# Optimization experiments

Measured on AMD Instinct MI355X. Metric: run time of the kernel, lower is better.

Reference implementation:

```python
import jax, jax.numpy as jnp
import numpy as np

B = 64        # number of jagged segments
LMAX = 1024   # max_seq_len
D = 512       # input feature dim
K = 512       # output feature dim
NW = 128      # number of selectable weight matrices
T = 32768     # total jagged tokens (avg len 512)


def setup_inputs() -> dict:
    rng = np.random.default_rng(0)
    # Monotone offsets with avg segment length T//B = 512, jittered +/-200
    # so every length stays in (0, LMAX].
    offsets = np.arange(B + 1, dtype=np.int64) * (T // B)
    offsets[1:-1] += rng.integers(-200, 200, size=B - 1)
    key = jax.random.key(0)
    k1, k2, k3, k4 = jax.random.split(key, 4)
    jagged = jax.random.normal(k1, (T, D), dtype=jnp.float32)
    weight = jax.random.normal(k2, (NW, D, K), dtype=jnp.float32) * 0.02
    bias = jax.random.normal(k3, (NW, K), dtype=jnp.float32)
    index = jax.random.randint(k4, (B,), 0, NW)
    return {
        "max_seq_len": LMAX,
        "offsets": jnp.asarray(offsets),
        "index": index,
        "jagged": jagged,
        "weight": weight,
        "bias": bias,
    }


def reference(max_seq_len, offsets, index, jagged, weight, bias):
    # out[offsets[b]:offsets[b+1]] = jagged[offsets[b]:offsets[b+1]] @ weight[index[b]] + bias[index[b]]
    T_, Dd = jagged.shape
    Kk = weight.shape[-1]
    starts = offsets[:-1]            # [B]
    ends = offsets[1:]               # [B]
    pos = starts[:, None] + jnp.arange(max_seq_len)[None, :]   # [B, L] global row ids
    valid = pos < ends[:, None]                                # [B, L]
    safe = jnp.where(valid, pos, 0)
    padded = jnp.where(valid[..., None], jagged[safe], 0)      # [B, L, D]
    w = weight[index]                                          # [B, D, K] (index-select)
    b = bias[index]                                            # [B, K]
    out_p = jnp.einsum("bld,bdk->blk", padded, w) + b[:, None, :]  # [B, L, K]
    # Scatter padded result back to jagged layout; invalid slots go to row T_ (dropped).
    scatter_idx = jnp.where(valid, pos, T_)
    out = jnp.zeros((T_ + 1, Kk), jagged.dtype).at[scatter_idx].set(out_p)
    return out[:T_]
```

## Files before the change

kernel.cpp:

```cpp
#include <hip/hip_runtime.h>
#include <hip/hip_bf16.h>

#define D_DIM 512
#define K_DIM 512
#define B_C   64
#define LMAX_C 1024

#define BM 128
#define BN 128
#define BK 64
#define KSTEPS 8
#define ROWT 8
#define COLT 4
#define NWG  (B_C * ROWT * COLT)

typedef __attribute__((ext_vector_type(8))) short bf16x8;
typedef __attribute__((ext_vector_type(4))) float f32x4;

__device__ __forceinline__ short f2bf(float f) {
    union { __hip_bfloat16 h; short s; } u;
    u.h = __float2bfloat16(f);
    return u.s;
}

__device__ __forceinline__ short* lds_addr(short* base, int row, int kbyte) {
    return (short*)((char*)base + row * 128 +
                    (kbyte ^ ((((row & 7) ^ ((row >> 2) & 7))) << 4)));
}

__global__ __launch_bounds__(256, 2) void jbmm_kernel(
    const int* __restrict__ offsets,
    const int* __restrict__ index,
    const float* __restrict__ jagged,
    const float* __restrict__ weight,
    const float* __restrict__ bias,
    float* __restrict__ out)
{
    __shared__ short As[2][BM * BK];
    __shared__ short Bs[2][BN * BK];

    const int bidRaw = blockIdx.x;
    const int bid = (bidRaw & 7) * (NWG / 8) + (bidRaw >> 3);

    const int b   = bid / (ROWT * COLT);
    const int rt  = (bid / COLT) % ROWT;
    const int ct  = bid % COLT;

    const int start = offsets[b];
    const int end   = offsets[b + 1];
    const int m0    = start + rt * BM;
    if (m0 >= end) return;
    const int rows = (end - m0) < BM ? (end - m0) : BM;

    const int idxw = index[b];
    const float* W = weight + (size_t)idxw * D_DIM * K_DIM;
    const int n0 = ct * BN;

    const int tid  = threadIdx.x;
    const int lane = tid & 63;
    const int wid  = tid >> 6;
    const int wr   = wid >> 1;
    const int wc   = wid & 1;
    const int lr   = lane & 15;
    const int lg   = lane >> 4;

    const int arow  = tid >> 3;
    const int acol8 = tid & 7;
    const int n4    = tid & 31;
    const int dq8   = tid >> 5;

    float bias_v[4];
#pragma unroll
    for (int ni = 0; ni < 4; ++ni)
        bias_v[ni] = bias[(size_t)idxw * K_DIM + n0 + wc * 64 + ni * 16 + lr];

    f32x4 acc[4][4];
#pragma unroll
    for (int mi = 0; mi < 4; ++mi)
#pragma unroll
        for (int ni = 0; ni < 4; ++ni)
            acc[mi][ni] = (f32x4){0.f, 0.f, 0.f, 0.f};

    f32x4 aR[8];
    f32x4 bR[8];

#define LOADA(k0_)                                                          \
    {                                                                       \
        _Pragma("unroll")                                                   \
        for (int i = 0; i < 4; ++i) {                                       \
            const int r = arow + 32 * i;                                    \
            f32x4 v0 = (f32x4){0.f,0.f,0.f,0.f};                            \
            f32x4 v1 = (f32x4){0.f,0.f,0.f,0.f};                            \
            if (r < rows) {                                                 \
                const float* p = &jagged[(size_t)(m0 + r) * D_DIM + (k0_) + acol8 * 8]; \
                v0 = *reinterpret_cast<const f32x4*>(p);                    \
                v1 = *reinterpret_cast<const f32x4*>(p + 4);                \
            }                                                               \
            aR[2 * i] = v0; aR[2 * i + 1] = v1;                             \
        }                                                                   \
    }

#define LOADB(k0_)                                                          \
    {                                                                       \
        _Pragma("unroll")                                                   \
        for (int j = 0; j < 8; ++j)                                         \
            bR[j] = *reinterpret_cast<const f32x4*>(                        \
                &W[(size_t)((k0_) + dq8 * 8 + j) * K_DIM + n0 + n4 * 4]);   \
    }

#define CVTSTORE(c_)                                                        \
    {                                                                       \
        _Pragma("unroll")                                                   \
        for (int i = 0; i < 4; ++i) {                                       \
            const int r = arow + 32 * i;                                    \
            bf16x8 w;                                                       \
            w[0] = f2bf(aR[2*i][0]); w[1] = f2bf(aR[2*i][1]);               \
            w[2] = f2bf(aR[2*i][2]); w[3] = f2bf(aR[2*i][3]);               \
            w[4] = f2bf(aR[2*i+1][0]); w[5] = f2bf(aR[2*i+1][1]);           \
            w[6] = f2bf(aR[2*i+1][2]); w[7] = f2bf(aR[2*i+1][3]);           \
            *reinterpret_cast<bf16x8*>(lds_addr(&As[c_][0], r, acol8 * 16)) = w; \
        }                                                                   \
        _Pragma("unroll")                                                   \
        for (int np = 0; np < 4; ++np) {                                    \
            bf16x8 w;                                                       \
            w[0] = f2bf(bR[0][np]); w[1] = f2bf(bR[1][np]);                 \
            w[2] = f2bf(bR[2][np]); w[3] = f2bf(bR[3][np]);                 \
            w[4] = f2bf(bR[4][np]); w[5] = f2bf(bR[5][np]);                 \
            w[6] = f2bf(bR[6][np]); w[7] = f2bf(bR[7][np]);                 \
            *reinterpret_cast<bf16x8*>(lds_addr(&Bs[c_][0], n4 * 4 + np, dq8 * 16)) = w; \
        }                                                                   \
    }

#define COMPUTE(c_)                                                         \
    {                                                                       \
        __builtin_amdgcn_s_setprio(1);                                      \
        _Pragma("unroll")                                                   \
        for (int kh = 0; kh < 2; ++kh) {                                    \
            bf16x8 af[4], bfr[4];                                           \
            _Pragma("unroll")                                               \
            for (int mi = 0; mi < 4; ++mi)                                  \
                af[mi] = *reinterpret_cast<bf16x8*>(                        \
                    lds_addr(&As[c_][0], wr * 64 + mi * 16 + lr, kh * 64 + lg * 16)); \
            _Pragma("unroll")                                               \
            for (int ni = 0; ni < 4; ++ni)                                  \
                bfr[ni] = *reinterpret_cast<bf16x8*>(                       \
                    lds_addr(&Bs[c_][0], wc * 64 + ni * 16 + lr, kh * 64 + lg * 16)); \
            _Pragma("unroll")                                               \
            for (int mi = 0; mi < 4; ++mi)                                  \
                _Pragma("unroll")                                           \
                for (int ni = 0; ni < 4; ++ni)                              \
                    acc[mi][ni] = __builtin_amdgcn_mfma_f32_16x16x32_bf16(  \
                        af[mi], bfr[ni], acc[mi][ni], 0, 0, 0);             \
        }                                                                   \
        __builtin_amdgcn_s_setprio(0);                                      \
    }

#define BARRIER_LDS()                                                       \
    {                                                                       \
        asm volatile("s_waitcnt lgkmcnt(0)" ::: "memory");                  \
        __builtin_amdgcn_s_barrier();                                       \
        asm volatile("" ::: "memory");                                      \
    }

    LOADA(0); LOADB(0);
    CVTSTORE(0);
    BARRIER_LDS();

#pragma unroll
    for (int t = 0; t < KSTEPS; ++t) {
        if (t + 1 < KSTEPS) {
            const int kn = (t + 1) * BK;
            LOADA(kn); LOADB(kn);
        }
        COMPUTE(t & 1);
        if (t + 1 < KSTEPS) {
            CVTSTORE((t + 1) & 1);
            BARRIER_LDS();
        }
    }

#pragma unroll
    for (int mi = 0; mi < 4; ++mi) {
        const int rloc = wr * 64 + mi * 16 + lg * 4;
#pragma unroll
        for (int r = 0; r < 4; ++r) {
            const int rr = rloc + r;
            if (rr < rows) {
#pragma unroll
                for (int ni = 0; ni < 4; ++ni) {
                    out[(size_t)(m0 + rr) * K_DIM + n0 + wc * 64 + ni * 16 + lr] =
                        acc[mi][ni][r] + bias_v[ni];
                }
            }
        }
    }
}

extern "C" void kernel_launch(void* const* d_in, const int* in_sizes, int n_in,
                              void* d_out, int out_size, void* d_ws, size_t ws_size,
                              hipStream_t stream) {
    const int*   offsets = (const int*)d_in[1];
    const int*   index   = (const int*)d_in[2];
    const float* jagged  = (const float*)d_in[3];
    const float* weight  = (const float*)d_in[4];
    const float* bias    = (const float*)d_in[5];
    float*       out     = (float*)d_out;

    dim3 grid(NWG);
    dim3 block(256);
    hipLaunchKernelGGL(jbmm_kernel, grid, block, 0, stream,
                       offsets, index, jagged, weight, bias, out);
}
```

Before: 46.56 us.

## Keep per-segment weight slice resident in LDS and loop over row tiles

Each workgroup now owns one (segment, column-tile) pair. It converts the full 512x128 weight slice to bf16 once into a 128KB LDS buffer, then loops over all row tiles of the segment, streaming only the activations through a double buffer. This removes the repeated fp32 weight loads and conversions that every row tile used to do. Block size goes to 512 threads, each wave owning a 64x32 output sub-tile. The cost is a grid of only 256 large workgroups with roughly 160KB of LDS each, so one fits per CU. Uneven segment lengths now become serial per-block imbalance, and there is less parallelism for hiding latency.

```diff
diff --git a/kernel.cpp b/kernel.cpp
--- a/kernel.cpp
+++ b/kernel.cpp
@@ -4,7 +4,6 @@
 #define D_DIM 512
 #define K_DIM 512
 #define B_C   64
-#define LMAX_C 1024
 
 #define BM 128
 #define BN 128
@@ -12,7 +11,7 @@
 #define KSTEPS 8
 #define ROWT 8
 #define COLT 4
-#define NWG  (B_C * ROWT * COLT)
+#define NWG  (B_C * COLT)
 
 typedef __attribute__((ext_vector_type(8))) short bf16x8;
 typedef __attribute__((ext_vector_type(4))) float f32x4;
@@ -23,12 +22,10 @@
     return u.s;
 }
 
-__device__ __forceinline__ short* lds_addr(short* base, int row, int kbyte) {
-    return (short*)((char*)base + row * 128 +
-                    (kbyte ^ ((((row & 7) ^ ((row >> 2) & 7))) << 4)));
-}
-
-__global__ __launch_bounds__(256, 2) void jbmm_kernel(
+__device__ __forceinline__ int fA(int r) { return (r & 7) ^ ((r >> 2) & 7); }
+__device__ __forceinline__ int fW(int r) { return (r & 15) ^ ((r >> 2) & 15); }
+
+__global__ __launch_bounds__(512, 2) void jbmm_kernel(
     const int* __restrict__ offsets,
     const int* __restrict__ index,
     const float* __restrict__ jagged,
@@ -36,119 +33,118 @@
     const float* __restrict__ bias,
     float* __restrict__ out)
 {
+    __shared__ short Ws[BN * D_DIM];
     __shared__ short As[2][BM * BK];
-    __shared__ short Bs[2][BN * BK];
 
     const int bidRaw = blockIdx.x;
     const int bid = (bidRaw & 7) * (NWG / 8) + (bidRaw >> 3);
-
-    const int b   = bid / (ROWT * COLT);
-    const int rt  = (bid / COLT) % ROWT;
-    const int ct  = bid % COLT;
+    const int b  = bid >> 2;
+    const int ct = bid & 3;
 
     const int start = offsets[b];
     const int end   = offsets[b + 1];
-    const int m0    = start + rt * BM;
-    if (m0 >= end) return;
-    const int rows = (end - m0) < BM ? (end - m0) : BM;
-
-    const int idxw = index[b];
-    const float* W = weight + (size_t)idxw * D_DIM * K_DIM;
-    const int n0 = ct * BN;
+    const int idxw  = index[b];
+    const int n0    = ct * BN;
+    const float* W  = weight + (size_t)idxw * D_DIM * K_DIM;
 
     const int tid  = threadIdx.x;
     const int lane = tid & 63;
     const int wid  = tid >> 6;
-    const int wr   = wid >> 1;
-    const int wc   = wid & 1;
+    const int wr   = wid >> 2;
+    const int wc   = wid & 3;
     const int lr   = lane & 15;
     const int lg   = lane >> 4;
 
-    const int arow  = tid >> 3;
-    const int acol8 = tid & 7;
-    const int n4    = tid & 31;
-    const int dq8   = tid >> 5;
-
-    float bias_v[4];
-#pragma unroll
-    for (int ni = 0; ni < 4; ++ni)
-        bias_v[ni] = bias[(size_t)idxw * K_DIM + n0 + wc * 64 + ni * 16 + lr];
-
-    f32x4 acc[4][4];
-#pragma unroll
-    for (int mi = 0; mi < 4; ++mi)
-#pragma unroll
-        for (int ni = 0; ni < 4; ++ni)
-            acc[mi][ni] = (f32x4){0.f, 0.f, 0.f, 0.f};
-
-    f32x4 aR[8];
-    f32x4 bR[8];
+    {
+        const int nq = tid & 31;
+        const int kg = tid >> 5;
+        for (int p = 0; p < 4; ++p) {
+            const int kbase = p * 128;
+            f32x4 wv[8];
+#pragma unroll
+            for (int j = 0; j < 8; ++j)
+                wv[j] = *reinterpret_cast<const f32x4*>(
+                    &W[(size_t)(kbase + kg * 8 + j) * K_DIM + n0 + nq * 4]);
+#pragma unroll
+            for (int np = 0; np < 4; ++np) {
+                const int row = nq * 4 + np;
+                bf16x8 w8;
+                w8[0] = f2bf(wv[0][np]); w8[1] = f2bf(wv[1][np]);
+                w8[2] = f2bf(wv[2][np]); w8[3] = f2bf(wv[3][np]);
+                w8[4] = f2bf(wv[4][np]); w8[5] = f2bf(wv[5][np]);
+                w8[6] = f2bf(wv[6][np]); w8[7] = f2bf(wv[7][np]);
+                const int sp = (p * 16 + kg) ^ fW(row);
+                *reinterpret_cast<bf16x8*>((char*)Ws + row * 1024 + sp * 16) = w8;
+            }
+        }
+    }
+
+    float bias_v[2];
+#pragma unroll
+    for (int ni = 0; ni < 2; ++ni)
+        bias_v[ni] = bias[(size_t)idxw * K_DIM + n0 + wc * 32 + ni * 16 + lr];
+
+    asm volatile("s_waitcnt lgkmcnt(0)" ::: "memory");
+    __builtin_amdgcn_s_barrier();
+    asm volatile("" ::: "memory");
+
+    const int arow  = tid >> 2;
+    const int acol4 = tid & 3;
+
+    f32x4 aR[4];
 
 #define LOADA(k0_)                                                          \
     {                                                                       \
+        if (arow < rows) {                                                  \
+            const float* p = &jagged[(size_t)(m0 + arow) * D_DIM + (k0_) + acol4 * 16]; \
+            _Pragma("unroll")                                               \
+            for (int j = 0; j < 4; ++j)                                     \
+                aR[j] = *reinterpret_cast<const f32x4*>(p + 4 * j);         \
+        } else {                                                            \
+            _Pragma("unroll")                                               \
+            for (int j = 0; j < 4; ++j)                                     \
+                aR[j] = (f32x4){0.f, 0.f, 0.f, 0.f};                        \
+        }                                                                   \
+    }
+
+#define CVTSTORE_A(c_)                                                      \
+    {                                                                       \
         _Pragma("unroll")                                                   \
-        for (int i = 0; i < 4; ++i) {                                       \
-            const int r = arow + 32 * i;                                    \
-            f32x4 v0 = (f32x4){0.f,0.f,0.f,0.f};                            \
-            f32x4 v1 = (f32x4){0.f,0.f,0.f,0.f};                            \
-            if (r < rows) {                                                 \
-                const float* p = &jagged[(size_t)(m0 + r) * D_DIM + (k0_) + acol8 * 8]; \
-                v0 = *reinterpret_cast<const f32x4*>(p);                    \
-                v1 = *reinterpret_cast<const f32x4*>(p + 4);                \
-            }                                                               \
-            aR[2 * i] = v0; aR[2 * i + 1] = v1;                             \
+        for (int j2 = 0; j2 < 2; ++j2) {                                    \
+            bf16x8 w8;                                                      \
+            w8[0] = f2bf(aR[2*j2][0]);   w8[1] = f2bf(aR[2*j2][1]);         \
+            w8[2] = f2bf(aR[2*j2][2]);   w8[3] = f2bf(aR[2*j2][3]);         \
+            w8[4] = f2bf(aR[2*j2+1][0]); w8[5] = f2bf(aR[2*j2+1][1]);       \
+            w8[6] = f2bf(aR[2*j2+1][2]); w8[7] = f2bf(aR[2*j2+1][3]);       \
+            const int sp = (acol4 * 2 + j2) ^ fA(arow);                     \
+            *reinterpret_cast<bf16x8*>((char*)&As[c_][0] + arow * 128 + sp * 16) = w8; \
         }                                                                   \
     }
 
-#define LOADB(k0_)                                                          \
-    {                                                                       \
-        _Pragma("unroll")                                                   \
-        for (int j = 0; j < 8; ++j)                                         \
-            bR[j] = *reinterpret_cast<const f32x4*>(                        \
-                &W[(size_t)((k0_) + dq8 * 8 + j) * K_DIM + n0 + n4 * 4]);   \
-    }
-
-#define CVTSTORE(c_)                                                        \
-    {                                                                       \
-        _Pragma("unroll")                                                   \
-        for (int i = 0; i < 4; ++i) {                                       \
-            const int r = arow + 32 * i;                                    \
-            bf16x8 w;                                                       \
-            w[0] = f2bf(aR[2*i][0]); w[1] = f2bf(aR[2*i][1]);               \
-            w[2] = f2bf(aR[2*i][2]); w[3] = f2bf(aR[2*i][3]);               \
-            w[4] = f2bf(aR[2*i+1][0]); w[5] = f2bf(aR[2*i+1][1]);           \
-            w[6] = f2bf(aR[2*i+1][2]); w[7] = f2bf(aR[2*i+1][3]);           \
-            *reinterpret_cast<bf16x8*>(lds_addr(&As[c_][0], r, acol8 * 16)) = w; \
-        }                                                                   \
-        _Pragma("unroll")                                                   \
-        for (int np = 0; np < 4; ++np) {                                    \
-            bf16x8 w;                                                       \
-            w[0] = f2bf(bR[0][np]); w[1] = f2bf(bR[1][np]);                 \
-            w[2] = f2bf(bR[2][np]); w[3] = f2bf(bR[3][np]);                 \
-            w[4] = f2bf(bR[4][np]); w[5] = f2bf(bR[5][np]);                 \
-            w[6] = f2bf(bR[6][np]); w[7] = f2bf(bR[7][np]);                 \
-            *reinterpret_cast<bf16x8*>(lds_addr(&Bs[c_][0], n4 * 4 + np, dq8 * 16)) = w; \
-        }                                                                   \
-    }
-
-#define COMPUTE(c_)                                                         \
+#define COMPUTE(c_, t_)                                                     \
     {                                                                       \
         __builtin_amdgcn_s_setprio(1);                                      \
         _Pragma("unroll")                                                   \
         for (int kh = 0; kh < 2; ++kh) {                                    \
-            bf16x8 af[4], bfr[4];                                           \
-            _Pragma("unroll")                                               \
-            for (int mi = 0; mi < 4; ++mi)                                  \
+            bf16x8 af[4], bfr[2];                                           \
+            _Pragma("unroll")                                               \
+            for (int mi = 0; mi < 4; ++mi) {                                \
+                const int row = wr * 64 + mi * 16 + lr;                     \
+                const int sp = (kh * 4 + lg) ^ fA(row);                     \
                 af[mi] = *reinterpret_cast<bf16x8*>(                        \
-                    lds_addr(&As[c_][0], wr * 64 + mi * 16 + lr, kh * 64 + lg * 16)); \
-            _Pragma("unroll")                                               \
-            for (int ni = 0; ni < 4; ++ni)                                  \
+                    (char*)&As[c_][0] + row * 128 + sp * 16);               \
+            }                                                               \
+            _Pragma("unroll")                                               \
+            for (int ni = 0; ni < 2; ++ni) {                                \
+                const int row = wc * 32 + ni * 16 + lr;                     \
+                const int sp = ((t_) * 8 + kh * 4 + lg) ^ fW(row);          \
                 bfr[ni] = *reinterpret_cast<bf16x8*>(                       \
-                    lds_addr(&Bs[c_][0], wc * 64 + ni * 16 + lr, kh * 64 + lg * 16)); \
+                    (char*)Ws + row * 1024 + sp * 16);                      \
+            }                                                               \
             _Pragma("unroll")                                               \
             for (int mi = 0; mi < 4; ++mi)                                  \
                 _Pragma("unroll")                                           \
-                for (int ni = 0; ni < 4; ++ni)                              \
+                for (int ni = 0; ni < 2; ++ni)                              \
                     acc[mi][ni] = __builtin_amdgcn_mfma_f32_16x16x32_bf16(  \
                         af[mi], bfr[ni], acc[mi][ni], 0, 0, 0);             \
         }                                                                   \
@@ -162,34 +158,43 @@
         asm volatile("" ::: "memory");                                      \
     }
 
-    LOADA(0); LOADB(0);
-    CVTSTORE(0);
-    BARRIER_LDS();
-
-#pragma unroll
-    for (int t = 0; t < KSTEPS; ++t) {
-        if (t + 1 < KSTEPS) {
-            const int kn = (t + 1) * BK;
-            LOADA(kn); LOADB(kn);
+    for (int rt = 0; rt < ROWT; ++rt) {
+        const int m0 = start + rt * BM;
+        if (m0 >= end) break;
+        const int rows = (end - m0) < BM ? (end - m0) : BM;
+
+        f32x4 acc[4][2];
+#pragma unroll
+        for (int mi = 0; mi < 4; ++mi)
+#pragma unroll
+            for (int ni = 0; ni < 2; ++ni)
+                acc[mi][ni] = (f32x4){0.f, 0.f, 0.f, 0.f};
+
+        LOADA(0);
+        CVTSTORE_A(0);
+        BARRIER_LDS();
+
+#pragma unroll
+        for (int t = 0; t < KSTEPS; ++t) {
+            if (t + 1 < KSTEPS) LOADA((t + 1) * BK);
+            COMPUTE(t & 1, t);
+            if (t + 1 < KSTEPS) {
+                CVTSTORE_A((t + 1) & 1);
+                BARRIER_LDS();
+            }
         }
-        COMPUTE(t & 1);
-        if (t + 1 < KSTEPS) {
-            CVTSTORE((t + 1) & 1);
-            BARRIER_LDS();
-        }
-    }
-
-#pragma unroll
-    for (int mi = 0; mi < 4; ++mi) {
-        const int rloc = wr * 64 + mi * 16 + lg * 4;
-#pragma unroll
-        for (int r = 0; r < 4; ++r) {
-            const int rr = rloc + r;
-            if (rr < rows) {
-#pragma unroll
-                for (int ni = 0; ni < 4; ++ni) {
-                    out[(size_t)(m0 + rr) * K_DIM + n0 + wc * 64 + ni * 16 + lr] =
-                        acc[mi][ni][r] + bias_v[ni];
+
+#pragma unroll
+        for (int mi = 0; mi < 4; ++mi) {
+            const int rbase = wr * 64 + mi * 16 + lg * 4;
+#pragma unroll
+            for (int r = 0; r < 4; ++r) {
+                const int rr = rbase + r;
+                if (rr < rows) {
+#pragma unroll
+                    for (int ni = 0; ni < 2; ++ni)
+                        out[(size_t)(m0 + rr) * K_DIM + n0 + wc * 32 + ni * 16 + lr] =
+                            acc[mi][ni][r] + bias_v[ni];
                 }
             }
         }
@@ -207,7 +212,7 @@
     float*       out     = (float*)d_out;
 
     dim3 grid(NWG);
-    dim3 block(256);
+    dim3 block(512);
     hipLaunchKernelGGL(jbmm_kernel, grid, block, 0, stream,
                        offsets, index, jagged, weight, bias, out);
 }
```

Result: slower. 68.47 us (+47.0%).

## Halve BK, deepen register prefetch to two stages, raise occupancy to three

Applied to the files above, without the earlier changes.

Cuts the K tile from 64 to 32 and doubles the number of K steps. Global loads now run two steps ahead, using a double-buffered register stage on top of the double-buffered LDS. The smaller LDS footprint allows launch_bounds occupancy of 3 blocks per CU, and a new 64-byte-row swizzle plus narrower load and store vectors fit the new tile shape. The aim is better latency hiding of the fp32 loads, at the cost of twice as many barriers, smaller vector loads for W, and more register pressure.

```diff
diff --git a/kernel.cpp b/kernel.cpp
--- a/kernel.cpp
+++ b/kernel.cpp
@@ -4,18 +4,19 @@
 #define D_DIM 512
 #define K_DIM 512
 #define B_C   64
-#define LMAX_C 1024
 
 #define BM 128
 #define BN 128
-#define BK 64
-#define KSTEPS 8
+#define BK 32
+#define KSTEPS 16
 #define ROWT 8
 #define COLT 4
 #define NWG  (B_C * ROWT * COLT)
 
 typedef __attribute__((ext_vector_type(8))) short bf16x8;
+typedef __attribute__((ext_vector_type(4))) short bf16x4;
 typedef __attribute__((ext_vector_type(4))) float f32x4;
+typedef __attribute__((ext_vector_type(2))) float f32x2;
 
 __device__ __forceinline__ short f2bf(float f) {
     union { __hip_bfloat16 h; short s; } u;
@@ -23,12 +24,11 @@
     return u.s;
 }
 
-__device__ __forceinline__ short* lds_addr(short* base, int row, int kbyte) {
-    return (short*)((char*)base + row * 128 +
-                    (kbyte ^ ((((row & 7) ^ ((row >> 2) & 7))) << 4)));
-}
-
-__global__ __launch_bounds__(256, 2) void jbmm_kernel(
+__device__ __forceinline__ char* lds_addr(short* base, int row, int slot, int byte_in_slot) {
+    return (char*)base + row * 64 + ((slot ^ ((row >> 1) & 3)) << 4) + byte_in_slot;
+}
+
+__global__ __launch_bounds__(256, 3) void jbmm_kernel(
     const int* __restrict__ offsets,
     const int* __restrict__ index,
     const float* __restrict__ jagged,
@@ -64,10 +64,10 @@
     const int lr   = lane & 15;
     const int lg   = lane >> 4;
 
-    const int arow  = tid >> 3;
-    const int acol8 = tid & 7;
-    const int n4    = tid & 31;
-    const int dq8   = tid >> 5;
+    const int arow = tid >> 3;
+    const int aq   = tid & 7;
+    const int wnp  = tid & 63;
+    const int wko  = tid >> 6;
 
     float bias_v[4];
 #pragma unroll
@@ -81,77 +81,72 @@
         for (int ni = 0; ni < 4; ++ni)
             acc[mi][ni] = (f32x4){0.f, 0.f, 0.f, 0.f};
 
-    f32x4 aR[8];
-    f32x4 bR[8];
-
-#define LOADA(k0_)                                                          \
+    f32x4 aR[2][4];
+    f32x2 bR[2][8];
+
+#define LOADA(k0_, s_)                                                      \
     {                                                                       \
         _Pragma("unroll")                                                   \
         for (int i = 0; i < 4; ++i) {                                       \
             const int r = arow + 32 * i;                                    \
-            f32x4 v0 = (f32x4){0.f,0.f,0.f,0.f};                            \
-            f32x4 v1 = (f32x4){0.f,0.f,0.f,0.f};                            \
-            if (r < rows) {                                                 \
-                const float* p = &jagged[(size_t)(m0 + r) * D_DIM + (k0_) + acol8 * 8]; \
-                v0 = *reinterpret_cast<const f32x4*>(p);                    \
-                v1 = *reinterpret_cast<const f32x4*>(p + 4);                \
-            }                                                               \
-            aR[2 * i] = v0; aR[2 * i + 1] = v1;                             \
+            f32x4 v = (f32x4){0.f, 0.f, 0.f, 0.f};                          \
+            if (r < rows)                                                   \
+                v = *reinterpret_cast<const f32x4*>(                        \
+                    &jagged[(size_t)(m0 + r) * D_DIM + (k0_) + aq * 4]);    \
+            aR[s_][i] = v;                                                  \
         }                                                                   \
     }
 
-#define LOADB(k0_)                                                          \
-    {                                                                       \
-        _Pragma("unroll")                                                   \
-        for (int j = 0; j < 8; ++j)                                         \
-            bR[j] = *reinterpret_cast<const f32x4*>(                        \
-                &W[(size_t)((k0_) + dq8 * 8 + j) * K_DIM + n0 + n4 * 4]);   \
-    }
-
-#define CVTSTORE(c_)                                                        \
+#define LOADB(k0_, s_)                                                      \
+    {                                                                       \
+        _Pragma("unroll")                                                   \
+        for (int jj = 0; jj < 8; ++jj)                                      \
+            bR[s_][jj] = *reinterpret_cast<const f32x2*>(                   \
+                &W[(size_t)((k0_) + wko * 8 + jj) * K_DIM + n0 + wnp * 2]); \
+    }
+
+#define CVTSTORE(s_, c_)                                                    \
     {                                                                       \
         _Pragma("unroll")                                                   \
         for (int i = 0; i < 4; ++i) {                                       \
             const int r = arow + 32 * i;                                    \
-            bf16x8 w;                                                       \
-            w[0] = f2bf(aR[2*i][0]); w[1] = f2bf(aR[2*i][1]);               \
-            w[2] = f2bf(aR[2*i][2]); w[3] = f2bf(aR[2*i][3]);               \
-            w[4] = f2bf(aR[2*i+1][0]); w[5] = f2bf(aR[2*i+1][1]);           \
-            w[6] = f2bf(aR[2*i+1][2]); w[7] = f2bf(aR[2*i+1][3]);           \
-            *reinterpret_cast<bf16x8*>(lds_addr(&As[c_][0], r, acol8 * 16)) = w; \
+            bf16x4 w4;                                                      \
+            w4[0] = f2bf(aR[s_][i][0]); w4[1] = f2bf(aR[s_][i][1]);         \
+            w4[2] = f2bf(aR[s_][i][2]); w4[3] = f2bf(aR[s_][i][3]);         \
+            *reinterpret_cast<bf16x4*>(                                     \
+                lds_addr(&As[c_][0], r, aq >> 1, (aq & 1) * 8)) = w4;       \
         }                                                                   \
         _Pragma("unroll")                                                   \
-        for (int np = 0; np < 4; ++np) {                                    \
-            bf16x8 w;                                                       \
-            w[0] = f2bf(bR[0][np]); w[1] = f2bf(bR[1][np]);                 \
-            w[2] = f2bf(bR[2][np]); w[3] = f2bf(bR[3][np]);                 \
-            w[4] = f2bf(bR[4][np]); w[5] = f2bf(bR[5][np]);                 \
-            w[6] = f2bf(bR[6][np]); w[7] = f2bf(bR[7][np]);                 \
-            *reinterpret_cast<bf16x8*>(lds_addr(&Bs[c_][0], n4 * 4 + np, dq8 * 16)) = w; \
+        for (int j = 0; j < 2; ++j) {                                       \
+            const int rb = wnp * 2 + j;                                     \
+            bf16x8 w8;                                                      \
+            w8[0] = f2bf(bR[s_][0][j]); w8[1] = f2bf(bR[s_][1][j]);         \
+            w8[2] = f2bf(bR[s_][2][j]); w8[3] = f2bf(bR[s_][3][j]);         \
+            w8[4] = f2bf(bR[s_][4][j]); w8[5] = f2bf(bR[s_][5][j]);         \
+            w8[6] = f2bf(bR[s_][6][j]); w8[7] = f2bf(bR[s_][7][j]);         \
+            *reinterpret_cast<bf16x8*>(                                     \
+                lds_addr(&Bs[c_][0], rb, wko, 0)) = w8;                     \
         }                                                                   \
     }
 
 #define COMPUTE(c_)                                                         \
     {                                                                       \
         __builtin_amdgcn_s_setprio(1);                                      \
-        _Pragma("unroll")                                                   \
-        for (int kh = 0; kh < 2; ++kh) {                                    \
-            bf16x8 af[4], bfr[4];                                           \
-            _Pragma("unroll")                                               \
-            for (int mi = 0; mi < 4; ++mi)                                  \
-                af[mi] = *reinterpret_cast<bf16x8*>(                        \
-                    lds_addr(&As[c_][0], wr * 64 + mi * 16 + lr, kh * 64 + lg * 16)); \
+        bf16x8 af[4], bfr[4];                                               \
+        _Pragma("unroll")                                                   \
+        for (int mi = 0; mi < 4; ++mi)                                      \
+            af[mi] = *reinterpret_cast<bf16x8*>(                            \
+                lds_addr(&As[c_][0], wr * 64 + mi * 16 + lr, lg, 0));       \
+        _Pragma("unroll")                                                   \
+        for (int ni = 0; ni < 4; ++ni)                                      \
+            bfr[ni] = *reinterpret_cast<bf16x8*>(                           \
+                lds_addr(&Bs[c_][0], wc * 64 + ni * 16 + lr, lg, 0));       \
+        _Pragma("unroll")                                                   \
+        for (int mi = 0; mi < 4; ++mi)                                      \
             _Pragma("unroll")                                               \
             for (int ni = 0; ni < 4; ++ni)                                  \
-                bfr[ni] = *reinterpret_cast<bf16x8*>(                       \
-                    lds_addr(&Bs[c_][0], wc * 64 + ni * 16 + lr, kh * 64 + lg * 16)); \
-            _Pragma("unroll")                                               \
-            for (int mi = 0; mi < 4; ++mi)                                  \
-                _Pragma("unroll")                                           \
-                for (int ni = 0; ni < 4; ++ni)                              \
-                    acc[mi][ni] = __builtin_amdgcn_mfma_f32_16x16x32_bf16(  \
-                        af[mi], bfr[ni], acc[mi][ni], 0, 0, 0);             \
-        }                                                                   \
+                acc[mi][ni] = __builtin_amdgcn_mfma_f32_16x16x32_bf16(      \
+                    af[mi], bfr[ni], acc[mi][ni], 0, 0, 0);                 \
         __builtin_amdgcn_s_setprio(0);                                      \
     }
 
@@ -162,19 +157,20 @@
         asm volatile("" ::: "memory");                                      \
     }
 
-    LOADA(0); LOADB(0);
-    CVTSTORE(0);
+    LOADA(0, 0); LOADB(0, 0);
+    LOADA(BK, 1); LOADB(BK, 1);
+    CVTSTORE(0, 0);
     BARRIER_LDS();
 
 #pragma unroll
     for (int t = 0; t < KSTEPS; ++t) {
-        if (t + 1 < KSTEPS) {
-            const int kn = (t + 1) * BK;
-            LOADA(kn); LOADB(kn);
+        if (t + 2 < KSTEPS) {
+            const int kn = (t + 2) * BK;
+            LOADA(kn, t & 1); LOADB(kn, t & 1);
         }
         COMPUTE(t & 1);
         if (t + 1 < KSTEPS) {
-            CVTSTORE((t + 1) & 1);
+            CVTSTORE((t + 1) & 1, (t + 1) & 1);
             BARRIER_LDS();
         }
     }
```

New measurement: 97.03 us. +108.4%, slower.

## Widen N tile to 256 and switch to single-buffered LDS staging

Applied to the files above, without the earlier changes.

Doubles the output tile width per workgroup (BN 128→256, COLT 4→2), so each jagged A tile is loaded and converted once per 256 columns instead of once per 128. LDS goes from double-buffered to single-buffered, with conversion fused straight into the global load. A second barrier is added before each stage, so global loads no longer overlap with MFMA compute. The change lowers redundant A traffic and grid size, but raises accumulator register pressure (32 f32x4 per thread) and serializes loads with compute.

```diff
diff --git a/kernel.cpp b/kernel.cpp
--- a/kernel.cpp
+++ b/kernel.cpp
@@ -4,14 +4,13 @@
 #define D_DIM 512
 #define K_DIM 512
 #define B_C   64
-#define LMAX_C 1024
 
 #define BM 128
-#define BN 128
+#define BN 256
 #define BK 64
 #define KSTEPS 8
 #define ROWT 8
-#define COLT 4
+#define COLT 2
 #define NWG  (B_C * ROWT * COLT)
 
 typedef __attribute__((ext_vector_type(8))) short bf16x8;
@@ -23,10 +22,7 @@
     return u.s;
 }
 
-__device__ __forceinline__ short* lds_addr(short* base, int row, int kbyte) {
-    return (short*)((char*)base + row * 128 +
-                    (kbyte ^ ((((row & 7) ^ ((row >> 2) & 7))) << 4)));
-}
+__device__ __forceinline__ int fS(int r) { return (r & 7) ^ ((r >> 2) & 7); }
 
 __global__ __launch_bounds__(256, 2) void jbmm_kernel(
     const int* __restrict__ offsets,
@@ -36,8 +32,8 @@
     const float* __restrict__ bias,
     float* __restrict__ out)
 {
-    __shared__ short As[2][BM * BK];
-    __shared__ short Bs[2][BN * BK];
+    __shared__ short As[BM * BK];
+    __shared__ short Bs[BN * BK];
 
     const int bidRaw = blockIdx.x;
     const int bid = (bidRaw & 7) * (NWG / 8) + (bidRaw >> 3);
@@ -66,26 +62,24 @@
 
     const int arow  = tid >> 3;
     const int acol8 = tid & 7;
-    const int n4    = tid & 31;
-    const int dq8   = tid >> 5;
+    const int nq    = tid & 63;
+    const int kg    = tid >> 6;
 
-    float bias_v[4];
+    float bias_v[8];
 #pragma unroll
-    for (int ni = 0; ni < 4; ++ni)
-        bias_v[ni] = bias[(size_t)idxw * K_DIM + n0 + wc * 64 + ni * 16 + lr];
+    for (int ni = 0; ni < 8; ++ni)
+        bias_v[ni] = bias[(size_t)idxw * K_DIM + n0 + wc * 128 + ni * 16 + lr];
 
-    f32x4 acc[4][4];
+    f32x4 acc[4][8];
 #pragma unroll
     for (int mi = 0; mi < 4; ++mi)
 #pragma unroll
-        for (int ni = 0; ni < 4; ++ni)
+        for (int ni = 0; ni < 8; ++ni)
             acc[mi][ni] = (f32x4){0.f, 0.f, 0.f, 0.f};
 
-    f32x4 aR[8];
-    f32x4 bR[8];
-
-#define LOADA(k0_)                                                          \
+#define STAGE(k0_)                                                          \
     {                                                                       \
+                                  \
         _Pragma("unroll")                                                   \
         for (int i = 0; i < 4; ++i) {                                       \
             const int r = arow + 32 * i;                                    \
@@ -96,61 +90,58 @@
                 v0 = *reinterpret_cast<const f32x4*>(p);                    \
                 v1 = *reinterpret_cast<const f32x4*>(p + 4);                \
             }                                                               \
-            aR[2 * i] = v0; aR[2 * i + 1] = v1;                             \
+            bf16x8 w8;                                                      \
+            w8[0] = f2bf(v0[0]); w8[1] = f2bf(v0[1]);                       \
+            w8[2] = f2bf(v0[2]); w8[3] = f2bf(v0[3]);                       \
+            w8[4] = f2bf(v1[0]); w8[5] = f2bf(v1[1]);                       \
+            w8[6] = f2bf(v1[2]); w8[7] = f2bf(v1[3]);                       \
+            *reinterpret_cast<bf16x8*>(                                     \
+                (char*)As + r * 128 + ((acol8 ^ fS(r)) << 4)) = w8;         \
+        }                                                                   \
+              \
+        _Pragma("unroll")                                                   \
+        for (int h = 0; h < 2; ++h) {                                       \
+            f32x4 bv[8];                                                    \
+            _Pragma("unroll")                                               \
+            for (int j = 0; j < 8; ++j)                                     \
+                bv[j] = *reinterpret_cast<const f32x4*>(                    \
+                    &W[(size_t)((k0_) + kg * 16 + h * 8 + j) * K_DIM + n0 + nq * 4]); \
+            _Pragma("unroll")                                               \
+            for (int np = 0; np < 4; ++np) {                                \
+                const int row = nq * 4 + np;                                \
+                bf16x8 w8;                                                  \
+                w8[0] = f2bf(bv[0][np]); w8[1] = f2bf(bv[1][np]);           \
+                w8[2] = f2bf(bv[2][np]); w8[3] = f2bf(bv[3][np]);           \
+                w8[4] = f2bf(bv[4][np]); w8[5] = f2bf(bv[5][np]);           \
+                w8[6] = f2bf(bv[6][np]); w8[7] = f2bf(bv[7][np]);           \
+                *reinterpret_cast<bf16x8*>(                                 \
+                    (char*)Bs + row * 128 + (((kg * 2 + h) ^ fS(row)) << 4)) = w8; \
+            }                                                               \
         }                                                                   \
     }
 
-#define LOADB(k0_)                                                          \
-    {                                                                       \
-        _Pragma("unroll")                                                   \
-        for (int j = 0; j < 8; ++j)                                         \
-            bR[j] = *reinterpret_cast<const f32x4*>(                        \
-                &W[(size_t)((k0_) + dq8 * 8 + j) * K_DIM + n0 + n4 * 4]);   \
-    }
-
-#define CVTSTORE(c_)                                                        \
-    {                                                                       \
-        _Pragma("unroll")                                                   \
-        for (int i = 0; i < 4; ++i) {                                       \
-            const int r = arow + 32 * i;                                    \
-            bf16x8 w;                                                       \
-            w[0] = f2bf(aR[2*i][0]); w[1] = f2bf(aR[2*i][1]);               \
-            w[2] = f2bf(aR[2*i][2]); w[3] = f2bf(aR[2*i][3]);               \
-            w[4] = f2bf(aR[2*i+1][0]); w[5] = f2bf(aR[2*i+1][1]);           \
-            w[6] = f2bf(aR[2*i+1][2]); w[7] = f2bf(aR[2*i+1][3]);           \
-            *reinterpret_cast<bf16x8*>(lds_addr(&As[c_][0], r, acol8 * 16)) = w; \
-        }                                                                   \
-        _Pragma("unroll")                                                   \
-        for (int np = 0; np < 4; ++np) {                                    \
-            bf16x8 w;                                                       \
-            w[0] = f2bf(bR[0][np]); w[1] = f2bf(bR[1][np]);                 \
-            w[2] = f2bf(bR[2][np]); w[3] = f2bf(bR[3][np]);                 \
-            w[4] = f2bf(bR[4][np]); w[5] = f2bf(bR[5][np]);                 \
-            w[6] = f2bf(bR[6][np]); w[7] = f2bf(bR[7][np]);                 \
-            *reinterpret_cast<bf16x8*>(lds_addr(&Bs[c_][0], n4 * 4 + np, dq8 * 16)) = w; \
-        }                                                                   \
-    }
-
-#define COMPUTE(c_)                                                         \
+#define COMPUTE()                                                           \
     {                                                                       \
         __builtin_amdgcn_s_setprio(1);                                      \
         _Pragma("unroll")                                                   \
         for (int kh = 0; kh < 2; ++kh) {                                    \
-            bf16x8 af[4], bfr[4];                                           \
+            bf16x8 af[4];                                                   \
             _Pragma("unroll")                                               \
-            for (int mi = 0; mi < 4; ++mi)                                  \
+            for (int mi = 0; mi < 4; ++mi) {                                \
+                const int row = wr * 64 + mi * 16 + lr;                     \
                 af[mi] = *reinterpret_cast<bf16x8*>(                        \
-                    lds_addr(&As[c_][0], wr * 64 + mi * 16 + lr, kh * 64 + lg * 16)); \
+                    (char*)As + row * 128 + (((kh * 4 + lg) ^ fS(row)) << 4)); \
+            }                                                               \
             _Pragma("unroll")                                               \
-            for (int ni = 0; ni < 4; ++ni)                                  \
-                bfr[ni] = *reinterpret_cast<bf16x8*>(                       \
-                    lds_addr(&Bs[c_][0], wc * 64 + ni * 16 + lr, kh * 64 + lg * 16)); \
-            _Pragma("unroll")                                               \
-            for (int mi = 0; mi < 4; ++mi)                                  \
+            for (int ni = 0; ni < 8; ++ni) {                                \
+                const int row = wc * 128 + ni * 16 + lr;                    \
+                bf16x8 bfr = *reinterpret_cast<bf16x8*>(                    \
+                    (char*)Bs + row * 128 + (((kh * 4 + lg) ^ fS(row)) << 4)); \
                 _Pragma("unroll")                                           \
-                for (int ni = 0; ni < 4; ++ni)                              \
+                for (int mi = 0; mi < 4; ++mi)                              \
                     acc[mi][ni] = __builtin_amdgcn_mfma_f32_16x16x32_bf16(  \
-                        af[mi], bfr[ni], acc[mi][ni], 0, 0, 0);             \
+                        af[mi], bfr, acc[mi][ni], 0, 0, 0);                 \
+            }                                                               \
         }                                                                   \
         __builtin_amdgcn_s_setprio(0);                                      \
     }
@@ -162,33 +153,28 @@
         asm volatile("" ::: "memory");                                      \
     }
 
-    LOADA(0); LOADB(0);
-    CVTSTORE(0);
+    STAGE(0);
     BARRIER_LDS();
-
 #pragma unroll
     for (int t = 0; t < KSTEPS; ++t) {
+        COMPUTE();
         if (t + 1 < KSTEPS) {
-            const int kn = (t + 1) * BK;
-            LOADA(kn); LOADB(kn);
-        }
-        COMPUTE(t & 1);
-        if (t + 1 < KSTEPS) {
-            CVTSTORE((t + 1) & 1);
+            BARRIER_LDS();
+            STAGE((t + 1) * BK);
             BARRIER_LDS();
         }
     }
 
 #pragma unroll
     for (int mi = 0; mi < 4; ++mi) {
-        const int rloc = wr * 64 + mi * 16 + lg * 4;
+        const int rbase = wr * 64 + mi * 16 + lg * 4;
 #pragma unroll
         for (int r = 0; r < 4; ++r) {
-            const int rr = rloc + r;
+            const int rr = rbase + r;
             if (rr < rows) {
 #pragma unroll
-                for (int ni = 0; ni < 4; ++ni) {
-                    out[(size_t)(m0 + rr) * K_DIM + n0 + wc * 64 + ni * 16 + lr] =
+                for (int ni = 0; ni < 8; ++ni) {
+                    out[(size_t)(m0 + rr) * K_DIM + n0 + wc * 128 + ni * 16 + lr] =
                         acc[mi][ni][r] + bias_v[ni];
                 }
             }
```

Result: slower. 118.6 us (+154.7%).
